# Performance work log

Measured on AMD Instinct MI355X. Metric: run time of the kernel, lower is better.

The kernel has to match this reference:

```python
import jax, jax.numpy as jnp
import numpy as np

NEG_INF = -1.0e10


def setup_inputs() -> dict:
    key = jax.random.key(0)
    ks = jax.random.split(key, 6)
    B, T, S = 64, 128, 512
    ENC, DEC = 1024, 512
    dec_hidden = jax.random.normal(ks[0], (B, T, DEC), dtype=jnp.float32)
    encoder_hiddens = jax.random.normal(ks[1], (B, S, ENC), dtype=jnp.float32)
    encoder_mask = jax.random.randint(ks[2], (B, S), 0, 2, dtype=jnp.int32)
    # nn.Linear(enc_dim, dec_dim) weight stored as [ENC, DEC] (already transposed)
    W_attn = jax.random.normal(ks[3], (ENC, DEC), dtype=jnp.float32) * (ENC ** -0.5)
    b_attn = jax.random.normal(ks[4], (DEC,), dtype=jnp.float32) * 0.01
    # linear_out: nn.Linear(enc_dim + dec_dim, dec_dim, bias=False)
    W_out = jax.random.normal(ks[5], (ENC + DEC, DEC), dtype=jnp.float32) * ((ENC + DEC) ** -0.5)
    return {
        "dec_hidden": dec_hidden,
        "encoder_hiddens": encoder_hiddens,
        "encoder_mask": encoder_mask,
        "W_attn": W_attn,
        "b_attn": b_attn,
        "W_out": W_out,
    }


def reference(dec_hidden, encoder_hiddens, encoder_mask, W_attn, b_attn, W_out):
    # --- score (method='general') ---
    maskf = encoder_mask.astype(dec_hidden.dtype)  # [B, S]
    proj = jnp.einsum("bse,ed->bsd", encoder_hiddens, W_attn) + b_attn  # [B, S, D]
    proj = proj * maskf[:, :, None]
    energies = jnp.einsum("btd,bsd->bts", dec_hidden, proj)  # [B, T, S]
    # --- mask-add + softmax ---
    neg_mask = NEG_INF * (1.0 - maskf)[:, None, :]  # [B, 1, S]
    masked_energies = energies + neg_mask
    attn_weights = jax.nn.softmax(masked_energies, axis=-1)  # [B, T, S]
    # --- weighted context + concat + linear_out + tanh ---
    weighted_context = jnp.einsum("bts,bse->bte", attn_weights, encoder_hiddens)
    h_cat = jnp.concatenate([weighted_context, dec_hidden], axis=-1)  # [B, T, E+D]
    h_tilde = jnp.tanh(jnp.einsum("btc,cd->btd", h_cat, W_out))  # [B, T, D]
    return h_tilde, attn_weights, masked_energies
```

## Files before the change

kernel.cpp:

```cpp
#include <hip/hip_runtime.h>
#include <cmath>

#define BB 64
#define TT 128
#define SS 512
#define EE 1024
#define DDIM 512
#define NEG_INF_F (-1.0e10f)

#define BM 128
#define BM2 64
#define BN 64
#define BK 32
#define LDSTP 20
#define ROWU 32

typedef unsigned short u16;
typedef __attribute__((ext_vector_type(8))) short bf16x8;
typedef __attribute__((ext_vector_type(4))) float f32x4;

__device__ __forceinline__ unsigned bf16_rne(float f) {
    unsigned u = __float_as_uint(f);
    return (u + 0x7fffu + ((u >> 16) & 1u)) >> 16;
}

__device__ __forceinline__ float fast_tanh(float x) {
    float t = __expf(-2.0f * fabsf(x));
    float r = __fdividef(1.0f - t, 1.0f + t);
    return copysignf(r, x);
}

template <int ROWS>
__device__ __forceinline__ void stage_glds(u16* lds, const u16* __restrict__ src,
                                           int ld, int tid) {
    const int w = tid >> 6, lane = tid & 63;
    const int rl = lane >> 2, p = lane & 3;
#pragma unroll
    for (int i = 0; i < ROWS / 64; ++i) {
        const int r0 = (w + 4 * i) * 16;
        const int r = r0 + rl;
        const int q = p ^ ((r >> 1) & 3);
        const u16* g = src + (size_t)r * ld + 8 * q;
        __builtin_amdgcn_global_load_lds(
            (const __attribute__((address_space(1))) unsigned*)g,
            (__attribute__((address_space(3))) unsigned*)(lds + r0 * ROWU),
            16, 0, 0);
    }
}

__device__ __forceinline__ bf16x8 read_frag_sw(const u16* buf, int row, int q) {
    const int c = q ^ ((row >> 1) & 3);
    return *(const bf16x8*)(buf + row * ROWU + 8 * c);
}

template <int ROWS>
__device__ __forceinline__ void stage_nt1(unsigned* hi,
                                          const float* __restrict__ src, int ld, int tid) {
#pragma unroll
    for (int i = 0; i < ROWS / 32; ++i) {
        int s = tid + 256 * i;
        int r = s >> 3, kq = s & 7;
        float4 v = *(const float4*)(src + (size_t)r * ld + 4 * kq);
        *(uint2*)&hi[r * LDSTP + 2 * kq] =
            make_uint2(bf16_rne(v.x) | (bf16_rne(v.y) << 16),
                       bf16_rne(v.z) | (bf16_rne(v.w) << 16));
    }
}

__device__ __forceinline__ void stage_tr1(unsigned* hi, const float* __restrict__ src,
                                          int ld, int tid) {
    int eq = tid & 15;
    int sp = tid >> 4;
    const float* p = src + (size_t)(2 * sp) * ld + 4 * eq;
    float4 va = *(const float4*)p;
    float4 vb = *(const float4*)(p + ld);
    float av[4] = {va.x, va.y, va.z, va.w};
    float bv[4] = {vb.x, vb.y, vb.z, vb.w};
#pragma unroll
    for (int c = 0; c < 4; ++c) {
        hi[(4 * eq + c) * LDSTP + sp] = bf16_rne(av[c]) | (bf16_rne(bv[c]) << 16);
    }
}

__device__ __forceinline__ bf16x8 read_frag_pad(const unsigned* buf, int row, int q) {
    return *(const bf16x8*)(buf + row * LDSTP + 4 * q);
}

__device__ __forceinline__ void mfma_ss1_64(const u16* Ah, const u16* Bh,
                                            f32x4 acc[2][2], int tid) {
    const int lane = tid & 63, w = tid >> 6;
    const int wm = (w & 1) * 32, wn = (w >> 1) * 32;
    const int fr = lane & 15, q = lane >> 4;
    bf16x8 ah[2];
#pragma unroll
    for (int i = 0; i < 2; ++i) ah[i] = read_frag_sw(Ah, wm + 16 * i + fr, q);
#pragma unroll
    for (int j = 0; j < 2; ++j) {
        bf16x8 bh = read_frag_sw(Bh, wn + 16 * j + fr, q);
#pragma unroll
        for (int i = 0; i < 2; ++i)
            acc[i][j] = __builtin_amdgcn_mfma_f32_16x16x32_bf16(ah[i], bh, acc[i][j], 0, 0, 0);
    }
}

__device__ __forceinline__ void mfma_sbp1_64(const u16* Ah, const unsigned* Bh,
                                             f32x4 acc[2][2], int tid) {
    const int lane = tid & 63, w = tid >> 6;
    const int wm = (w & 1) * 32, wn = (w >> 1) * 32;
    const int fr = lane & 15, q = lane >> 4;
    bf16x8 ah[2];
#pragma unroll
    for (int i = 0; i < 2; ++i) ah[i] = read_frag_sw(Ah, wm + 16 * i + fr, q);
#pragma unroll
    for (int j = 0; j < 2; ++j) {
        bf16x8 bh = read_frag_pad(Bh, wn + 16 * j + fr, q);
#pragma unroll
        for (int i = 0; i < 2; ++i)
            acc[i][j] = __builtin_amdgcn_mfma_f32_16x16x32_bf16(ah[i], bh, acc[i][j], 0, 0, 0);
    }
}

__device__ __forceinline__ void mfma_sp1(const u16* Ah, const unsigned* Bh,
                                         f32x4 acc[4][2], int tid) {
    const int lane = tid & 63, w = tid >> 6;
    const int wm = (w & 1) * 64, wn = (w >> 1) * 32;
    const int fr = lane & 15, q = lane >> 4;
    bf16x8 ah[4];
#pragma unroll
    for (int i = 0; i < 4; ++i) ah[i] = read_frag_sw(Ah, wm + 16 * i + fr, q);
#pragma unroll
    for (int j = 0; j < 2; ++j) {
        bf16x8 bh = read_frag_pad(Bh, wn + 16 * j + fr, q);
#pragma unroll
        for (int i = 0; i < 4; ++i)
            acc[i][j] = __builtin_amdgcn_mfma_f32_16x16x32_bf16(ah[i], bh, acc[i][j], 0, 0, 0);
    }
}

__device__ __forceinline__ void mfma_s1(const u16* Ah, const u16* Bh,
                                        f32x4 acc[4][2], int tid) {
    const int lane = tid & 63, w = tid >> 6;
    const int wm = (w & 1) * 64, wn = (w >> 1) * 32;
    const int fr = lane & 15, q = lane >> 4;
    bf16x8 ah[4];
#pragma unroll
    for (int i = 0; i < 4; ++i) ah[i] = read_frag_sw(Ah, wm + 16 * i + fr, q);
#pragma unroll
    for (int j = 0; j < 2; ++j) {
        bf16x8 bh = read_frag_sw(Bh, wn + 16 * j + fr, q);
#pragma unroll
        for (int i = 0; i < 4; ++i)
            acc[i][j] = __builtin_amdgcn_mfma_f32_16x16x32_bf16(ah[i], bh, acc[i][j], 0, 0, 0);
    }
}

__global__ __launch_bounds__(256) void k_conv1(const float* __restrict__ src,
                                               u16* __restrict__ hi) {
    const int i = blockIdx.x * 256 + threadIdx.x;
    float4 v = ((const float4*)src)[i];
    ((ushort4*)hi)[i] = make_ushort4((u16)bf16_rne(v.x), (u16)bf16_rne(v.y),
                                     (u16)bf16_rne(v.z), (u16)bf16_rne(v.w));
}

__global__ __launch_bounds__(256) void k_wot(const float* __restrict__ Wo,
                                             u16* __restrict__ thi) {
    __shared__ float t[64][65];
    const int tid = threadIdx.x;
    const int r0 = blockIdx.x * 64;
    const int c0 = blockIdx.y * 64;
    const int rr = tid >> 4, cc = tid & 15;
#pragma unroll
    for (int i = 0; i < 4; ++i) {
        float4 v = *(const float4*)(Wo + (size_t)(r0 + rr + 16 * i) * DDIM + c0 + 4 * cc);
        t[rr + 16 * i][4 * cc + 0] = v.x;
        t[rr + 16 * i][4 * cc + 1] = v.y;
        t[rr + 16 * i][4 * cc + 2] = v.z;
        t[rr + 16 * i][4 * cc + 3] = v.w;
    }
    __syncthreads();
#pragma unroll
    for (int i = 0; i < 4; ++i) {
        const int oc = rr + 16 * i;
        size_t off = (size_t)(c0 + oc) * (EE + DDIM) + r0 + 4 * cc;
        *(ushort4*)(thi + off) = make_ushort4((u16)bf16_rne(t[4 * cc + 0][oc]),
                                              (u16)bf16_rne(t[4 * cc + 1][oc]),
                                              (u16)bf16_rne(t[4 * cc + 2][oc]),
                                              (u16)bf16_rne(t[4 * cc + 3][oc]));
    }
}

__global__ __launch_bounds__(256) void k_decw(const u16* __restrict__ Ahp,
                                              const u16* __restrict__ Bhp,
                                              u16* __restrict__ Chi) {
    __shared__ u16 Ah[2][BM2 * ROWU], Bh[2][BN * ROWU];
    const int tid = threadIdx.x;
    const int bm = blockIdx.x * BM2, bn = blockIdx.y * BN;
    f32x4 acc[2][2] = {};
    for (int k0 = 0; k0 < DDIM; k0 += 2 * BK) {
        __syncthreads();
        stage_glds<BM2>(Ah[0], Ahp + (size_t)bm * DDIM + k0, DDIM, tid);
        stage_glds<BM2>(Ah[1], Ahp + (size_t)bm * DDIM + k0 + BK, DDIM, tid);
        stage_glds<BN>(Bh[0], Bhp + (size_t)bn * DDIM + k0, DDIM, tid);
        stage_glds<BN>(Bh[1], Bhp + (size_t)bn * DDIM + k0 + BK, DDIM, tid);
        __builtin_amdgcn_s_waitcnt(0);
        __syncthreads();
        mfma_ss1_64(Ah[0], Bh[0], acc, tid);
        mfma_ss1_64(Ah[1], Bh[1], acc, tid);
    }
    const int lane = tid & 63, w = tid >> 6;
    const int wm = (w & 1) * 32, wn = (w >> 1) * 32;
    const int fr = lane & 15, q = lane >> 4;
#pragma unroll
    for (int j = 0; j < 2; ++j) {
        const int col = bn + wn + 16 * j + fr;
#pragma unroll
        for (int i = 0; i < 2; ++i)
#pragma unroll
            for (int r = 0; r < 4; ++r) {
                const int row = bm + wm + 16 * i + 4 * q + r;
                Chi[(size_t)row * EE + col] = (u16)bf16_rne(acc[i][j][r]);
            }
    }
}

__global__ __launch_bounds__(256) void k_decb(const float* __restrict__ dec,
                                              const float* __restrict__ ba,
                                              float* __restrict__ decb) {
    const int row = blockIdx.x * 4 + (threadIdx.x >> 6);
    const int lane = threadIdx.x & 63;
    const float* x = dec + (size_t)row * DDIM;
    float s = 0.f;
#pragma unroll
    for (int i = 0; i < 8; ++i) {
        int idx = lane + i * 64;
        s += x[idx] * ba[idx];
    }
#pragma unroll
    for (int off = 32; off >= 1; off >>= 1) s += __shfl_xor(s, off, 64);
    if (lane == 0) decb[row] = s;
}

__global__ __launch_bounds__(256) void k_energy(const u16* __restrict__ Ahp,
                                                const float* __restrict__ enc,
                                                const int* __restrict__ mask,
                                                const float* __restrict__ decb,
                                                float* __restrict__ menerg) {
    const int b = blockIdx.z;
    const int bn = blockIdx.x * BN;
    const int bm = blockIdx.y * BM2;
    __shared__ u16 Ah[2][BM2 * ROWU];
    __shared__ unsigned Bh[2][BN * LDSTP];
    const int tid = threadIdx.x;
    const u16* Abh = Ahp + (size_t)b * TT * EE + (size_t)bm * EE;
    const float* Bt = enc + (size_t)b * SS * EE + (size_t)bn * EE;
    f32x4 acc[2][2] = {};
    for (int k0 = 0; k0 < EE; k0 += 2 * BK) {
        __syncthreads();
        stage_glds<BM2>(Ah[0], Abh + k0, EE, tid);
        stage_glds<BM2>(Ah[1], Abh + k0 + BK, EE, tid);
        stage_nt1<BN>(Bh[0], Bt + k0, EE, tid);
        stage_nt1<BN>(Bh[1], Bt + k0 + BK, EE, tid);
        __builtin_amdgcn_s_waitcnt(0);
        __syncthreads();
        mfma_sbp1_64(Ah[0], Bh[0], acc, tid);
        mfma_sbp1_64(Ah[1], Bh[1], acc, tid);
    }
    const int lane = tid & 63, w = tid >> 6;
    const int wm = (w & 1) * 32, wn = (w >> 1) * 32;
    const int fr = lane & 15, q = lane >> 4;
    const int* mb = mask + (size_t)b * SS;
    const float* dbp = decb + (size_t)b * TT + bm;
    float* Crow = menerg + (size_t)b * TT * SS + (size_t)bm * SS;
    float db[2][4];
#pragma unroll
    for (int i = 0; i < 2; ++i) {
        float4 d4 = *(const float4*)(dbp + wm + 16 * i + 4 * q);
        db[i][0] = d4.x; db[i][1] = d4.y; db[i][2] = d4.z; db[i][3] = d4.w;
    }
#pragma unroll
    for (int j = 0; j < 2; ++j) {
        const int col = bn + wn + 16 * j + fr;
        const int mk = mb[col];
#pragma unroll
        for (int i = 0; i < 2; ++i)
#pragma unroll
            for (int r = 0; r < 4; ++r) {
                const int row = wm + 16 * i + 4 * q + r;
                Crow[(size_t)row * SS + col] = mk ? acc[i][j][r] + db[i][r] : NEG_INF_F;
            }
    }
}

__global__ __launch_bounds__(128) void k_softmax(const float* __restrict__ me,
                                                 float* __restrict__ attn,
                                                 u16* __restrict__ ahi) {
    const int row = blockIdx.x;
    const int tid = threadIdx.x;
    const float4 v = ((const float4*)(me + (size_t)row * SS))[tid];
    float m = fmaxf(fmaxf(v.x, v.y), fmaxf(v.z, v.w));
#pragma unroll
    for (int off = 32; off >= 1; off >>= 1) m = fmaxf(m, __shfl_xor(m, off, 64));
    __shared__ float redm[2];
    __shared__ float reds[2];
    const int wv = tid >> 6, lane = tid & 63;
    if (lane == 0) redm[wv] = m;
    __syncthreads();
    m = fmaxf(redm[0], redm[1]);
    float e0 = __expf(v.x - m), e1 = __expf(v.y - m);
    float e2 = __expf(v.z - m), e3 = __expf(v.w - m);
    float s = (e0 + e1) + (e2 + e3);
#pragma unroll
    for (int off = 32; off >= 1; off >>= 1) s += __shfl_xor(s, off, 64);
    if (lane == 0) reds[wv] = s;
    __syncthreads();
    s = reds[0] + reds[1];
    const float inv = 1.0f / s;
    float o0 = e0 * inv, o1 = e1 * inv, o2 = e2 * inv, o3 = e3 * inv;
    ((float4*)(attn + (size_t)row * SS))[tid] = make_float4(o0, o1, o2, o3);
    ((ushort4*)(ahi + (size_t)row * SS))[tid] =
        make_ushort4((u16)bf16_rne(o0), (u16)bf16_rne(o1),
                     (u16)bf16_rne(o2), (u16)bf16_rne(o3));
}

__global__ __launch_bounds__(256) void k_ctx(const u16* __restrict__ Ahp,
                                             const float* __restrict__ enc,
                                             u16* __restrict__ Chi) {
    const int b = blockIdx.z;
    const int bn = blockIdx.x * BN;
    __shared__ u16 Ah[2][BM * ROWU];
    __shared__ unsigned Bh[2][BN * LDSTP];
    const int tid = threadIdx.x;
    const u16* Abh = Ahp + (size_t)b * TT * SS;
    const float* Bm = enc + (size_t)b * SS * EE + bn;
    f32x4 acc[4][2] = {};
    for (int k0 = 0; k0 < SS; k0 += 2 * BK) {
        __syncthreads();
        stage_glds<BM>(Ah[0], Abh + k0, SS, tid);
        stage_glds<BM>(Ah[1], Abh + k0 + BK, SS, tid);
        stage_tr1(Bh[0], Bm + (size_t)k0 * EE, EE, tid);
        stage_tr1(Bh[1], Bm + (size_t)(k0 + BK) * EE, EE, tid);
        __builtin_amdgcn_s_waitcnt(0);
        __syncthreads();
        mfma_sp1(Ah[0], Bh[0], acc, tid);
        mfma_sp1(Ah[1], Bh[1], acc, tid);
    }
    const int lane = tid & 63, w = tid >> 6;
    const int wm = (w & 1) * 64, wn = (w >> 1) * 32;
    const int fr = lane & 15, q = lane >> 4;
    u16* Ch = Chi + (size_t)b * TT * EE;
#pragma unroll
    for (int j = 0; j < 2; ++j) {
        const int col = bn + wn + 16 * j + fr;
#pragma unroll
        for (int i = 0; i < 4; ++i)
#pragma unroll
            for (int r = 0; r < 4; ++r) {
                const int row = wm + 16 * i + 4 * q + r;
                Ch[(size_t)row * EE + col] = (u16)bf16_rne(acc[i][j][r]);
            }
    }
}

__global__ __launch_bounds__(256) void k_out(const u16* __restrict__ wch,
                                             const u16* __restrict__ dech,
                                             const u16* __restrict__ woth,
                                             float* __restrict__ ht) {
    __shared__ u16 Ah[2][BM * ROWU], Bh[2][BN * ROWU];
    const int tid = threadIdx.x;
    const int bm = blockIdx.x * BM, bn = blockIdx.y * BN;
    const int KTOT = EE + DDIM;
    f32x4 acc[4][2] = {};
    for (int k0 = 0; k0 < KTOT; k0 += 2 * BK) {
        __syncthreads();
#pragma unroll
        for (int s = 0; s < 2; ++s) {
            const int kk = k0 + BK * s;
            const u16* ah;
            int ld;
            if (kk < EE) {
                ah = wch + (size_t)bm * EE + kk;
                ld = EE;
            } else {
                ah = dech + (size_t)bm * DDIM + (kk - EE);
                ld = DDIM;
            }
            stage_glds<BM>(Ah[s], ah, ld, tid);
            stage_glds<BN>(Bh[s], woth + (size_t)bn * KTOT + kk, KTOT, tid);
        }
        __builtin_amdgcn_s_waitcnt(0);
        __syncthreads();
        mfma_s1(Ah[0], Bh[0], acc, tid);
        mfma_s1(Ah[1], Bh[1], acc, tid);
    }
    const int lane = tid & 63, w = tid >> 6;
    const int wm = (w & 1) * 64, wn = (w >> 1) * 32;
    const int fr = lane & 15, q = lane >> 4;
#pragma unroll
    for (int j = 0; j < 2; ++j) {
        const int col = bn + wn + 16 * j + fr;
#pragma unroll
        for (int i = 0; i < 4; ++i)
#pragma unroll
            for (int r = 0; r < 4; ++r) {
                const int row = bm + wm + 16 * i + 4 * q + r;
                ht[(size_t)row * DDIM + col] = fast_tanh(acc[i][j][r]);
            }
    }
}

extern "C" void kernel_launch(void* const* d_in, const int* in_sizes, int n_in,
                              void* d_out, int out_size, void* d_ws, size_t ws_size,
                              hipStream_t stream) {
    (void)in_sizes; (void)n_in; (void)out_size; (void)ws_size;
    const float* dec = (const float*)d_in[0];
    const float* enc = (const float*)d_in[1];
    const int* mask = (const int*)d_in[2];
    const float* Wa = (const float*)d_in[3];
    const float* ba = (const float*)d_in[4];
    const float* Wo = (const float*)d_in[5];

    float* h_tilde = (float*)d_out;
    float* attn = h_tilde + (size_t)BB * TT * DDIM;
    float* menerg = attn + (size_t)BB * TT * SS;

    char* ws = (char*)d_ws;
    u16* decW_hi = (u16*)(ws);
    u16* dec_hi  = (u16*)(ws + 33554432);
    u16* attn_hi = (u16*)(ws + 50331648);
    u16* wa_hi   = (u16*)(ws + 67108864);
    u16* wot_hi  = (u16*)(ws + 69206016);
    float* decb  = (float*)(ws + 72351744);
    u16* wc_hi = decW_hi;

    k_conv1<<<(BB * TT * DDIM) / 4 / 256, 256, 0, stream>>>(dec, dec_hi);
    k_conv1<<<(EE * DDIM) / 4 / 256, 256, 0, stream>>>(Wa, wa_hi);
    k_wot<<<dim3((EE + DDIM) / 64, DDIM / 64), 256, 0, stream>>>(Wo, wot_hi);
    k_decb<<<(BB * TT) / 4, 256, 0, stream>>>(dec, ba, decb);
    k_decw<<<dim3((BB * TT) / BM2, EE / BN), 256, 0, stream>>>(dec_hi, wa_hi, decW_hi);
    k_energy<<<dim3(SS / BN, TT / BM2, BB), 256, 0, stream>>>(decW_hi, enc, mask, decb, menerg);
    k_softmax<<<BB * TT, 128, 0, stream>>>(menerg, attn, attn_hi);
    k_ctx<<<dim3(EE / BN, 1, BB), 256, 0, stream>>>(attn_hi, enc, wc_hi);
    k_out<<<dim3((BB * TT) / BM, DDIM / BN), 256, 0, stream>>>(wc_hi, dec_hi, wot_hi, h_tilde);
}
```

Measured before the change: 328.4 us.

## Double-buffer LDS staging with prefetch in all four GEMM kernels

Converts the GEMM kernels (decw, energy, ctx, out) from a load-wait-compute loop into a two-stage software pipeline. The next K tile is fetched into the other LDS buffer while the current one feeds MFMA, using partial vmcnt waits and sched barriers. For the fp32 enc operand, global loads go into registers first and are packed to bf16 into LDS after compute. This is meant to hide global memory latency, at the cost of twice the LDS footprint (which may lower occupancy) and more live registers.

```diff
diff --git a/kernel.cpp b/kernel.cpp
--- a/kernel.cpp
+++ b/kernel.cpp
@@ -18,6 +18,23 @@
 typedef unsigned short u16;
 typedef __attribute__((ext_vector_type(8))) short bf16x8;
 typedef __attribute__((ext_vector_type(4))) float f32x4;
+
+#define SBAR()                                  \
+    do {                                        \
+        __builtin_amdgcn_sched_barrier(0);      \
+        __builtin_amdgcn_s_barrier();           \
+        __builtin_amdgcn_sched_barrier(0);      \
+    } while (0)
+#define WAITVM(N)                                                   \
+    do {                                                            \
+        asm volatile("s_waitcnt vmcnt(" #N ")" ::: "memory");       \
+        __builtin_amdgcn_sched_barrier(0);                          \
+    } while (0)
+#define WAITLGKM()                                                  \
+    do {                                                            \
+        asm volatile("s_waitcnt lgkmcnt(0)" ::: "memory");          \
+        __builtin_amdgcn_sched_barrier(0);                          \
+    } while (0)
 
 __device__ __forceinline__ unsigned bf16_rne(float f) {
     unsigned u = __float_as_uint(f);
@@ -53,29 +70,39 @@
     return *(const bf16x8*)(buf + row * ROWU + 8 * c);
 }
 
-template <int ROWS>
-__device__ __forceinline__ void stage_nt1(unsigned* hi,
-                                          const float* __restrict__ src, int ld, int tid) {
-#pragma unroll
-    for (int i = 0; i < ROWS / 32; ++i) {
+__device__ __forceinline__ void nt_load(float4* v, const float* __restrict__ src,
+                                        int ld, int tid) {
+#pragma unroll
+    for (int i = 0; i < 2; ++i) {
         int s = tid + 256 * i;
         int r = s >> 3, kq = s & 7;
-        float4 v = *(const float4*)(src + (size_t)r * ld + 4 * kq);
+        v[i] = *(const float4*)(src + (size_t)r * ld + 4 * kq);
+    }
+}
+__device__ __forceinline__ void nt_pack(unsigned* hi, const float4* v, int tid) {
+#pragma unroll
+    for (int i = 0; i < 2; ++i) {
+        int s = tid + 256 * i;
+        int r = s >> 3, kq = s & 7;
         *(uint2*)&hi[r * LDSTP + 2 * kq] =
-            make_uint2(bf16_rne(v.x) | (bf16_rne(v.y) << 16),
-                       bf16_rne(v.z) | (bf16_rne(v.w) << 16));
-    }
-}
-
-__device__ __forceinline__ void stage_tr1(unsigned* hi, const float* __restrict__ src,
-                                          int ld, int tid) {
+            make_uint2(bf16_rne(v[i].x) | (bf16_rne(v[i].y) << 16),
+                       bf16_rne(v[i].z) | (bf16_rne(v[i].w) << 16));
+    }
+}
+
+__device__ __forceinline__ void tr_load(float4* v, const float* __restrict__ src,
+                                        int ld, int tid) {
     int eq = tid & 15;
     int sp = tid >> 4;
     const float* p = src + (size_t)(2 * sp) * ld + 4 * eq;
-    float4 va = *(const float4*)p;
-    float4 vb = *(const float4*)(p + ld);
-    float av[4] = {va.x, va.y, va.z, va.w};
-    float bv[4] = {vb.x, vb.y, vb.z, vb.w};
+    v[0] = *(const float4*)p;
+    v[1] = *(const float4*)(p + ld);
+}
+__device__ __forceinline__ void tr_pack(unsigned* hi, const float4* v, int tid) {
+    int eq = tid & 15;
+    int sp = tid >> 4;
+    float av[4] = {v[0].x, v[0].y, v[0].z, v[0].w};
+    float bv[4] = {v[1].x, v[1].y, v[1].z, v[1].w};
 #pragma unroll
     for (int c = 0; c < 4; ++c) {
         hi[(4 * eq + c) * LDSTP + sp] = bf16_rne(av[c]) | (bf16_rne(bv[c]) << 16);
@@ -192,20 +219,41 @@
 __global__ __launch_bounds__(256) void k_decw(const u16* __restrict__ Ahp,
                                               const u16* __restrict__ Bhp,
                                               u16* __restrict__ Chi) {
-    __shared__ u16 Ah[2][BM2 * ROWU], Bh[2][BN * ROWU];
+    __shared__ u16 Ah[2][2 * BM2 * ROWU], Bh[2][2 * BN * ROWU];
     const int tid = threadIdx.x;
     const int bm = blockIdx.x * BM2, bn = blockIdx.y * BN;
+    const u16* As = Ahp + (size_t)bm * DDIM;
+    const u16* Bs = Bhp + (size_t)bn * DDIM;
     f32x4 acc[2][2] = {};
-    for (int k0 = 0; k0 < DDIM; k0 += 2 * BK) {
-        __syncthreads();
-        stage_glds<BM2>(Ah[0], Ahp + (size_t)bm * DDIM + k0, DDIM, tid);
-        stage_glds<BM2>(Ah[1], Ahp + (size_t)bm * DDIM + k0 + BK, DDIM, tid);
-        stage_glds<BN>(Bh[0], Bhp + (size_t)bn * DDIM + k0, DDIM, tid);
-        stage_glds<BN>(Bh[1], Bhp + (size_t)bn * DDIM + k0 + BK, DDIM, tid);
-        __builtin_amdgcn_s_waitcnt(0);
-        __syncthreads();
-        mfma_ss1_64(Ah[0], Bh[0], acc, tid);
-        mfma_ss1_64(Ah[1], Bh[1], acc, tid);
+    const int NT = DDIM / (2 * BK);
+
+    stage_glds<BM2>(&Ah[0][0], As, DDIM, tid);
+    stage_glds<BM2>(&Ah[0][BM2 * ROWU], As + BK, DDIM, tid);
+    stage_glds<BN>(&Bh[0][0], Bs, DDIM, tid);
+    stage_glds<BN>(&Bh[0][BN * ROWU], Bs + BK, DDIM, tid);
+
+    for (int t = 0; t < NT - 1; ++t) {
+        const int k1 = (t + 1) * 2 * BK;
+        const int bf = (t + 1) & 1;
+        stage_glds<BM2>(&Ah[bf][0], As + k1, DDIM, tid);
+        stage_glds<BM2>(&Ah[bf][BM2 * ROWU], As + k1 + BK, DDIM, tid);
+        stage_glds<BN>(&Bh[bf][0], Bs + k1, DDIM, tid);
+        stage_glds<BN>(&Bh[bf][BN * ROWU], Bs + k1 + BK, DDIM, tid);
+        WAITVM(4);
+        SBAR();
+        const u16* a = Ah[t & 1];
+        const u16* b = Bh[t & 1];
+        mfma_ss1_64(a, b, acc, tid);
+        mfma_ss1_64(a + BM2 * ROWU, b + BN * ROWU, acc, tid);
+        SBAR();
+    }
+    WAITVM(0);
+    SBAR();
+    {
+        const u16* a = Ah[(NT - 1) & 1];
+        const u16* b = Bh[(NT - 1) & 1];
+        mfma_ss1_64(a, b, acc, tid);
+        mfma_ss1_64(a + BM2 * ROWU, b + BN * ROWU, acc, tid);
     }
     const int lane = tid & 63, w = tid >> 6;
     const int wm = (w & 1) * 32, wn = (w >> 1) * 32;
@@ -248,22 +296,49 @@
     const int b = blockIdx.z;
     const int bn = blockIdx.x * BN;
     const int bm = blockIdx.y * BM2;
-    __shared__ u16 Ah[2][BM2 * ROWU];
-    __shared__ unsigned Bh[2][BN * LDSTP];
+    __shared__ u16 Ah[2][2 * BM2 * ROWU];
+    __shared__ unsigned Bp[2][2 * BN * LDSTP];
     const int tid = threadIdx.x;
     const u16* Abh = Ahp + (size_t)b * TT * EE + (size_t)bm * EE;
     const float* Bt = enc + (size_t)b * SS * EE + (size_t)bn * EE;
     f32x4 acc[2][2] = {};
-    for (int k0 = 0; k0 < EE; k0 += 2 * BK) {
-        __syncthreads();
-        stage_glds<BM2>(Ah[0], Abh + k0, EE, tid);
-        stage_glds<BM2>(Ah[1], Abh + k0 + BK, EE, tid);
-        stage_nt1<BN>(Bh[0], Bt + k0, EE, tid);
-        stage_nt1<BN>(Bh[1], Bt + k0 + BK, EE, tid);
-        __builtin_amdgcn_s_waitcnt(0);
-        __syncthreads();
-        mfma_sbp1_64(Ah[0], Bh[0], acc, tid);
-        mfma_sbp1_64(Ah[1], Bh[1], acc, tid);
+    float4 bv[4];
+    const int NT = EE / (2 * BK);
+
+    nt_load(&bv[0], Bt, EE, tid);
+    nt_load(&bv[2], Bt + BK, EE, tid);
+    stage_glds<BM2>(&Ah[0][0], Abh, EE, tid);
+    stage_glds<BM2>(&Ah[0][BM2 * ROWU], Abh + BK, EE, tid);
+    nt_pack(&Bp[0][0], &bv[0], tid);
+    nt_pack(&Bp[0][BN * LDSTP], &bv[2], tid);
+    WAITLGKM();
+
+    for (int t = 0; t < NT - 1; ++t) {
+        const int k1 = (t + 1) * 2 * BK;
+        const int bf = (t + 1) & 1;
+        nt_load(&bv[0], Bt + k1, EE, tid);
+        nt_load(&bv[2], Bt + k1 + BK, EE, tid);
+        stage_glds<BM2>(&Ah[bf][0], Abh + k1, EE, tid);
+        stage_glds<BM2>(&Ah[bf][BM2 * ROWU], Abh + k1 + BK, EE, tid);
+        WAITVM(6);
+        SBAR();
+        const u16* a = Ah[t & 1];
+        const unsigned* bb = Bp[t & 1];
+        mfma_sbp1_64(a, bb, acc, tid);
+        mfma_sbp1_64(a + BM2 * ROWU, bb + BN * LDSTP, acc, tid);
+        __builtin_amdgcn_sched_barrier(0);
+        nt_pack(&Bp[bf][0], &bv[0], tid);
+        nt_pack(&Bp[bf][BN * LDSTP], &bv[2], tid);
+        WAITLGKM();
+        SBAR();
+    }
+    WAITVM(0);
+    SBAR();
+    {
+        const u16* a = Ah[(NT - 1) & 1];
+        const unsigned* bb = Bp[(NT - 1) & 1];
+        mfma_sbp1_64(a, bb, acc, tid);
+        mfma_sbp1_64(a + BM2 * ROWU, bb + BN * LDSTP, acc, tid);
     }
     const int lane = tid & 63, w = tid >> 6;
     const int wm = (w & 1) * 32, wn = (w >> 1) * 32;
@@ -327,22 +402,49 @@
                                              u16* __restrict__ Chi) {
     const int b = blockIdx.z;
     const int bn = blockIdx.x * BN;
-    __shared__ u16 Ah[2][BM * ROWU];
-    __shared__ unsigned Bh[2][BN * LDSTP];
+    __shared__ u16 Ah[2][2 * BM * ROWU];
+    __shared__ unsigned Bp[2][2 * BN * LDSTP];
     const int tid = threadIdx.x;
     const u16* Abh = Ahp + (size_t)b * TT * SS;
     const float* Bm = enc + (size_t)b * SS * EE + bn;
     f32x4 acc[4][2] = {};
-    for (int k0 = 0; k0 < SS; k0 += 2 * BK) {
-        __syncthreads();
-        stage_glds<BM>(Ah[0], Abh + k0, SS, tid);
-        stage_glds<BM>(Ah[1], Abh + k0 + BK, SS, tid);
-        stage_tr1(Bh[0], Bm + (size_t)k0 * EE, EE, tid);
-        stage_tr1(Bh[1], Bm + (size_t)(k0 + BK) * EE, EE, tid);
-        __builtin_amdgcn_s_waitcnt(0);
-        __syncthreads();
-        mfma_sp1(Ah[0], Bh[0], acc, tid);
-        mfma_sp1(Ah[1], Bh[1], acc, tid);
+    float4 bv0[2], bv1[2];
+    const int NT = SS / (2 * BK);
+
+    tr_load(bv0, Bm, EE, tid);
+    tr_load(bv1, Bm + (size_t)BK * EE, EE, tid);
+    stage_glds<BM>(&Ah[0][0], Abh, SS, tid);
+    stage_glds<BM>(&Ah[0][BM * ROWU], Abh + BK, SS, tid);
+    tr_pack(&Bp[0][0], bv0, tid);
+    tr_pack(&Bp[0][BN * LDSTP], bv1, tid);
+    WAITLGKM();
+
+    for (int t = 0; t < NT - 1; ++t) {
+        const int k1 = (t + 1) * 2 * BK;
+        const int bf = (t + 1) & 1;
+        tr_load(bv0, Bm + (size_t)k1 * EE, EE, tid);
+        tr_load(bv1, Bm + (size_t)(k1 + BK) * EE, EE, tid);
+        stage_glds<BM>(&Ah[bf][0], Abh + k1, SS, tid);
+        stage_glds<BM>(&Ah[bf][BM * ROWU], Abh + k1 + BK, SS, tid);
+        WAITVM(8);
+        SBAR();
+        const u16* a = Ah[t & 1];
+        const unsigned* bb = Bp[t & 1];
+        mfma_sp1(a, bb, acc, tid);
+        mfma_sp1(a + BM * ROWU, bb + BN * LDSTP, acc, tid);
+        __builtin_amdgcn_sched_barrier(0);
+        tr_pack(&Bp[bf][0], bv0, tid);
+        tr_pack(&Bp[bf][BN * LDSTP], bv1, tid);
+        WAITLGKM();
+        SBAR();
+    }
+    WAITVM(0);
+    SBAR();
+    {
+        const u16* a = Ah[(NT - 1) & 1];
+        const unsigned* bb = Bp[(NT - 1) & 1];
+        mfma_sp1(a, bb, acc, tid);
+        mfma_sp1(a + BM * ROWU, bb + BN * LDSTP, acc, tid);
     }
     const int lane = tid & 63, w = tid >> 6;
     const int wm = (w & 1) * 64, wn = (w >> 1) * 32;
@@ -365,13 +467,14 @@
                                              const u16* __restrict__ dech,
                                              const u16* __restrict__ woth,
                                              float* __restrict__ ht) {
-    __shared__ u16 Ah[2][BM * ROWU], Bh[2][BN * ROWU];
+    __shared__ u16 Ah[2][2 * BM * ROWU], Bh[2][2 * BN * ROWU];
     const int tid = threadIdx.x;
     const int bm = blockIdx.x * BM, bn = blockIdx.y * BN;
     const int KTOT = EE + DDIM;
     f32x4 acc[4][2] = {};
-    for (int k0 = 0; k0 < KTOT; k0 += 2 * BK) {
-        __syncthreads();
+    const int NT = KTOT / (2 * BK);
+
+    auto STG = [&](int k0, int bf) {
 #pragma unroll
         for (int s = 0; s < 2; ++s) {
             const int kk = k0 + BK * s;
@@ -384,13 +487,29 @@
                 ah = dech + (size_t)bm * DDIM + (kk - EE);
                 ld = DDIM;
             }
-            stage_glds<BM>(Ah[s], ah, ld, tid);
-            stage_glds<BN>(Bh[s], woth + (size_t)bn * KTOT + kk, KTOT, tid);
+            stage_glds<BM>(&Ah[bf][s * BM * ROWU], ah, ld, tid);
+            stage_glds<BN>(&Bh[bf][s * BN * ROWU], woth + (size_t)bn * KTOT + kk, KTOT, tid);
         }
-        __builtin_amdgcn_s_waitcnt(0);
-        __syncthreads();
-        mfma_s1(Ah[0], Bh[0], acc, tid);
-        mfma_s1(Ah[1], Bh[1], acc, tid);
+    };
+
+    STG(0, 0);
+    for (int t = 0; t < NT - 1; ++t) {
+        STG((t + 1) * 2 * BK, (t + 1) & 1);
+        WAITVM(6);
+        SBAR();
+        const u16* a = Ah[t & 1];
+        const u16* b = Bh[t & 1];
+        mfma_s1(a, b, acc, tid);
+        mfma_s1(a + BM * ROWU, b + BN * ROWU, acc, tid);
+        SBAR();
+    }
+    WAITVM(0);
+    SBAR();
+    {
+        const u16* a = Ah[(NT - 1) & 1];
+        const u16* b = Bh[(NT - 1) & 1];
+        mfma_s1(a, b, acc, tid);
+        mfma_s1(a + BM * ROWU, b + BN * ROWU, acc, tid);
     }
     const int lane = tid & 63, w = tid >> 6;
     const int wm = (w & 1) * 64, wn = (w >> 1) * 32;
```

Measured after the change: 331.9 us. No clear change (+1.1%).
